# Optimization experiments

Hardware: AMD Instinct MI355X
Metric: run time of the kernel (lower is better)

Reference implementation:

```python
import jax, jax.numpy as jnp
import numpy as np

N_E = 1024
E_DIM = 256
DECAY = 0.99
BETA = 1.0
EPS = 1e-5


def setup_inputs() -> dict:
    key = jax.random.key(0)
    k1, k2, k3 = jax.random.split(key, 3)
    z = jax.random.normal(k1, (32, E_DIM, 64, 64), dtype=jnp.float32)
    embedding = jax.random.normal(k2, (N_E, E_DIM), dtype=jnp.float32)
    embedding_avg = embedding  # buffers initialized as clone of embedding
    cluster_size = jnp.ones((N_E,), dtype=jnp.float32)
    return {"z": z, "embedding": embedding, "embedding_avg": embedding_avg,
            "cluster_size": cluster_size}


def reference(z, embedding, embedding_avg, cluster_size):
    B, C, H, W = z.shape
    zp = jnp.transpose(z, (0, 2, 3, 1))          # [B,H,W,C]
    zf = zp.reshape(-1, C)                        # [N,C]

    # squared euclidean distances [N, n_e]
    d = (jnp.sum(zf * zf, axis=1, keepdims=True)
         + jnp.sum(embedding * embedding, axis=1)[None, :]
         - 2.0 * zf @ embedding.T)
    idx = jnp.argmin(d, axis=1)                   # [N]

    z_q = embedding[idx].reshape(zp.shape)        # [B,H,W,C] (old codebook)

    # training-mode EMA update (scatter-based accumulation)
    counts = jnp.zeros((N_E,), dtype=zf.dtype).at[idx].add(1.0)
    emb_sum = jnp.zeros((N_E, C), dtype=zf.dtype).at[idx].add(zf)
    new_cluster_size = cluster_size * DECAY + (1.0 - DECAY) * counts
    new_embedding_avg = embedding_avg * DECAY + (1.0 - DECAY) * emb_sum
    n = jnp.sum(new_cluster_size)
    smoothed = (new_cluster_size + EPS) / (n + N_E * EPS) * n
    new_embedding = new_embedding_avg / smoothed[:, None]

    sg = jax.lax.stop_gradient
    loss = (BETA * jnp.mean((sg(z_q) - zp) ** 2)
            + jnp.mean((z_q - sg(zp)) ** 2))

    z_q_st = zp + sg(z_q - zp)                    # straight-through
    z_q_out = jnp.transpose(z_q_st, (0, 3, 1, 2))  # back to NCHW
    min_encoding_indices = idx.reshape(B, H, W)
    return (z_q_out, loss, min_encoding_indices,
            new_embedding, new_embedding_avg, new_cluster_size)
```

## Files before the change

### kernel.cpp

```cpp
#include <hip/hip_runtime.h>

#define BATCH 32
#define CDIM 256
#define HW 4096
#define NVEC 131072
#define NE 1024
#define DECAY 0.99f
#define ONE_MINUS_DECAY 0.01f
#define EPSV 1e-5f
#define ZQ_ELEMS 33554432
#define MARGIN 0.02f

typedef _Float16 half8 __attribute__((ext_vector_type(8)));
typedef _Float16 half4 __attribute__((ext_vector_type(4)));
typedef float    f32x4 __attribute__((ext_vector_type(4)));

__global__ __launch_bounds__(256) void prep_half_kernel(
    const float* __restrict__ emb, _Float16* __restrict__ embH,
    _Float16* __restrict__ embL) {
  int i = blockIdx.x * 256 + threadIdx.x;
  float4 v = ((const float4*)emb)[i];
  float x[4] = {v.x, v.y, v.z, v.w};
  half4 hv, lv;
  #pragma unroll
  for (int j = 0; j < 4; ++j) {
    _Float16 h = (_Float16)x[j];
    hv[j] = h;
    lv[j] = (_Float16)(x[j] - (float)h);
  }
  *(half4*)(embH + 4 * (size_t)i) = hv;
  *(half4*)(embL + 4 * (size_t)i) = lv;
}

__global__ __launch_bounds__(256) void enorm_kernel(
    const float* __restrict__ emb, float* __restrict__ enorm) {
  int gid  = blockIdx.x * 256 + threadIdx.x;
  int e    = gid >> 6;
  int lane = threadIdx.x & 63;
  const float4* row = (const float4*)(emb + ((size_t)e << 8));
  float4 v = row[lane];
  float s = v.x * v.x + v.y * v.y + v.z * v.z + v.w * v.w;
  #pragma unroll
  for (int off = 32; off > 0; off >>= 1) s += __shfl_down(s, off);
  if (lane == 0) enorm[e] = s;
}

__global__ __launch_bounds__(512, 2) void argmin_kernel(
    const float* __restrict__ z, const _Float16* __restrict__ embH,
    const _Float16* __restrict__ embL, const float* __restrict__ enorm,
    int* __restrict__ idx_ws, float* __restrict__ idx_out,
    float* __restrict__ counts, int* __restrict__ flag_cnt,
    int* __restrict__ flag_list) {
  __shared__ char smem[65536];

  const int t = threadIdx.x;
  const int w = t >> 6;
  const int l = t & 63;
  const int g = l >> 4;
  const int c = l & 15;
  const int wn = w >> 2;
  const int we = w & 3;

  const int n0  = blockIdx.x * 64;
  const int b   = n0 >> 12;
  const int hw0 = n0 & 4095;
  const float* zb = z + ((size_t)b << 20) + hw0;

  {
    const int n  = t & 63;
    const int kg = t >> 6;
    char* zhp = smem;
    char* zlp = smem + 32768;
    #pragma unroll
    for (int it = 0; it < 4; ++it) {
      const int k0 = it * 64 + kg * 8;
      half8 hv, lv;
      #pragma unroll
      for (int j = 0; j < 8; ++j) {
        float x = zb[(size_t)(k0 + j) * HW + n];
        _Float16 h = (_Float16)x;
        hv[j] = h;
        lv[j] = (_Float16)(x - (float)h);
      }
      const int slot = ((k0 >> 3) ^ (n & 31)) & 31;
      const int byte = n * 512 + slot * 16;
      *(half8*)(zhp + byte) = hv;
      *(half8*)(zlp + byte) = lv;
    }
  }
  __syncthreads();

  float bd[2][4];
  int   bi[2][4];
  unsigned amb = 0u;
  #pragma unroll
  for (int mi = 0; mi < 2; ++mi)
    #pragma unroll
    for (int r = 0; r < 4; ++r) { bd[mi][r] = 3.0e38f; bi[mi][r] = 0; }

  int arow[2], axor[2];
  #pragma unroll
  for (int mi = 0; mi < 2; ++mi) {
    int rowm = 32 * wn + 16 * mi + c;
    arow[mi] = rowm * 512;
    axor[mi] = rowm & 31;
  }

  const char* bhp = (const char*)embH;
  const char* blp = (const char*)embL;

  #pragma unroll 1
  for (int et = 0; et < 4; ++et) {
    const int ebase = et * 256 + we * 64;
    f32x4 acc[2][4];
    #pragma unroll
    for (int mi = 0; mi < 2; ++mi)
      #pragma unroll
      for (int ni = 0; ni < 4; ++ni) {
        f32x4 zr = {0.0f, 0.0f, 0.0f, 0.0f};
        acc[mi][ni] = zr;
      }

    int boff[4];
    #pragma unroll
    for (int ni = 0; ni < 4; ++ni) {
      int eg = ebase + 16 * ni + c;
      boff[ni] = eg * 512 + g * 16;
    }

    #pragma unroll 2
    for (int kc = 0; kc < 256; kc += 32) {
      half8 ah[2], al[2];
      const int kslot = (kc >> 3) + g;
      #pragma unroll
      for (int mi = 0; mi < 2; ++mi) {
        int byte = arow[mi] + (((kslot ^ axor[mi]) & 31) << 4);
        ah[mi] = *(const half8*)(smem + byte);
        al[mi] = *(const half8*)(smem + 32768 + byte);
      }
      #pragma unroll
      for (int nh = 0; nh < 2; ++nh) {
        half8 bh0, bl0, bh1, bl1;
        {
          int o0 = boff[2 * nh]     + kc * 2;
          int o1 = boff[2 * nh + 1] + kc * 2;
          bh0 = *(const half8*)(bhp + o0);
          bl0 = *(const half8*)(blp + o0);
          bh1 = *(const half8*)(bhp + o1);
          bl1 = *(const half8*)(blp + o1);
        }
        #pragma unroll
        for (int mi = 0; mi < 2; ++mi) {
          acc[mi][2*nh]   = __builtin_amdgcn_mfma_f32_16x16x32_f16(ah[mi], bh0, acc[mi][2*nh],   0, 0, 0);
          acc[mi][2*nh]   = __builtin_amdgcn_mfma_f32_16x16x32_f16(ah[mi], bl0, acc[mi][2*nh],   0, 0, 0);
          acc[mi][2*nh]   = __builtin_amdgcn_mfma_f32_16x16x32_f16(al[mi], bh0, acc[mi][2*nh],   0, 0, 0);
          acc[mi][2*nh+1] = __builtin_amdgcn_mfma_f32_16x16x32_f16(ah[mi], bh1, acc[mi][2*nh+1], 0, 0, 0);
          acc[mi][2*nh+1] = __builtin_amdgcn_mfma_f32_16x16x32_f16(ah[mi], bl1, acc[mi][2*nh+1], 0, 0, 0);
          acc[mi][2*nh+1] = __builtin_amdgcn_mfma_f32_16x16x32_f16(al[mi], bh1, acc[mi][2*nh+1], 0, 0, 0);
        }
      }
    }

    #pragma unroll
    for (int ni = 0; ni < 4; ++ni) {
      const int e = ebase + 16 * ni + c;
      const float en = enorm[e];
      #pragma unroll
      for (int mi = 0; mi < 2; ++mi)
        #pragma unroll
        for (int r = 0; r < 4; ++r) {
          const unsigned bit = 1u << (mi * 4 + r);
          float old = bd[mi][r];
          float d = en - 2.0f * acc[mi][ni][r];
          bool better = d < old;
          bool nearr  = fabsf(d - old) < MARGIN;
          if (better) { bd[mi][r] = d; bi[mi][r] = e; }
          unsigned nb = better ? (nearr ? bit : 0u)
                               : ((amb & bit) | (nearr ? bit : 0u));
          amb = (amb & ~bit) | nb;
        }
    }
  }

  #pragma unroll
  for (int off = 1; off < 16; off <<= 1) {
    unsigned oamb = __shfl_xor(amb, off);
    unsigned namb = 0u;
    #pragma unroll
    for (int mi = 0; mi < 2; ++mi)
      #pragma unroll
      for (int r = 0; r < 4; ++r) {
        const unsigned bit = 1u << (mi * 4 + r);
        float od = __shfl_xor(bd[mi][r], off);
        int   oi = __shfl_xor(bi[mi][r], off);
        bool nearr = fabsf(od - bd[mi][r]) < MARGIN;
        bool ow = (od < bd[mi][r]) || (od == bd[mi][r] && oi < bi[mi][r]);
        unsigned sel = ow ? (oamb & bit) : (amb & bit);
        if (ow) { bd[mi][r] = od; bi[mi][r] = oi; }
        if (nearr) sel |= bit;
        namb |= sel;
      }
    amb = namb;
  }

  __syncthreads();
  float* sd = (float*)smem;
  int*   si = (int*)(smem + 1024);
  int*   sa = (int*)(smem + 2048);
  if (c == 0) {
    #pragma unroll
    for (int mi = 0; mi < 2; ++mi)
      #pragma unroll
      for (int r = 0; r < 4; ++r) {
        int nloc = 16 * mi + 4 * g + r;
        sd[w * 32 + nloc] = bd[mi][r];
        si[w * 32 + nloc] = bi[mi][r];
        sa[w * 32 + nloc] = (int)((amb >> (mi * 4 + r)) & 1u);
      }
  }
  __syncthreads();
  if (t < 64) {
    const int half = t >> 5;
    const int rloc = t & 31;
    const int base = half * 128 + rloc;
    float d = sd[base]; int i = si[base]; int a = sa[base];
    #pragma unroll
    for (int j = 1; j < 4; ++j) {
      float od = sd[base + j * 32];
      int   oi = si[base + j * 32];
      int   oa = sa[base + j * 32];
      bool nearr = fabsf(od - d) < MARGIN;
      bool ow = (od < d) || (od == d && oi < i);
      a = (ow ? oa : a) | (nearr ? 1 : 0);
      if (ow) { d = od; i = oi; }
    }
    const int n = n0 + t;
    idx_ws[n]  = i;
    idx_out[n] = (float)i;
    atomicAdd(&counts[i], 1.0f);
    if (a) {
      int p = atomicAdd(flag_cnt, 1);
      flag_list[p] = n;
    }
  }
}

__global__ __launch_bounds__(256) void fixup_kernel(
    const float* __restrict__ z, const float* __restrict__ emb,
    const float* __restrict__ enorm, const int* __restrict__ flag_cnt,
    const int* __restrict__ flag_list, int* __restrict__ idx_ws,
    float* __restrict__ idx_out, float* __restrict__ counts) {
  __shared__ float zf[256];
  __shared__ float rd[256];
  __shared__ int   ri[256];
  const int t = threadIdx.x;
  const int cnt = *flag_cnt;
  for (int fi = blockIdx.x; fi < cnt; fi += gridDim.x) {
    const int n = flag_list[fi];
    const int b = n >> 12, hw = n & 4095;
    __syncthreads();
    zf[t] = z[((size_t)b << 20) + ((size_t)t << 12) + hw];
    __syncthreads();
    float bdv = 3.0e38f; int biv = 0;
    #pragma unroll 1
    for (int rep = 0; rep < 4; ++rep) {
      const int e = rep * 256 + t;
      const float4* er = (const float4*)(emb + ((size_t)e << 8));
      const float4* zr = (const float4*)zf;
      float d0 = 0.f, d1 = 0.f, d2 = 0.f, d3 = 0.f;
      #pragma unroll 8
      for (int k4 = 0; k4 < 64; ++k4) {
        float4 ev = er[k4];
        float4 zv = zr[k4];
        d0 = fmaf(ev.x, zv.x, d0);
        d1 = fmaf(ev.y, zv.y, d1);
        d2 = fmaf(ev.z, zv.z, d2);
        d3 = fmaf(ev.w, zv.w, d3);
      }
      float d = enorm[e] - 2.0f * ((d0 + d1) + (d2 + d3));
      if (d < bdv) { bdv = d; biv = e; }
    }
    rd[t] = bdv; ri[t] = biv;
    __syncthreads();
    for (int s = 128; s > 0; s >>= 1) {
      if (t < s) {
        float od = rd[t + s]; int oi = ri[t + s];
        if (od < rd[t] || (od == rd[t] && oi < ri[t])) { rd[t] = od; ri[t] = oi; }
      }
      __syncthreads();
    }
    if (t == 0) {
      const int nw  = ri[0];
      const int old = idx_ws[n];
      if (nw != old) {
        atomicAdd(&counts[old], -1.0f);
        atomicAdd(&counts[nw],  1.0f);
        idx_ws[n]  = nw;
        idx_out[n] = (float)nw;
      }
    }
    __syncthreads();
  }
}

__global__ __launch_bounds__(256) void fused_scatter_kernel(
    const float* __restrict__ z, const float* __restrict__ emb,
    const int* __restrict__ idx_ws, float* __restrict__ zq_out,
    float* __restrict__ loss_acc, float* __restrict__ emb_sum) {
  __shared__ float hist[NE];
  int t = threadIdx.x;
  #pragma unroll
  for (int i = t; i < NE; i += 256) hist[i] = 0.0f;
  __syncthreads();

  int c     = blockIdx.x & 255;
  int chunk = blockIdx.x >> 8;
  int base  = chunk << 14;

  float lsum = 0.0f;
  const int4* idx4 = (const int4*)idx_ws;
  for (int i4 = t; i4 < 4096; i4 += 256) {
    int n0 = base + (i4 << 2);
    int b  = n0 >> 12;
    int hw = n0 & 4095;
    size_t off = (((size_t)(b << 8) + c) << 12) + hw;
    float4 v = *(const float4*)(z + off);
    int4 id = idx4[n0 >> 2];
    float4 q;
    q.x = emb[((size_t)id.x << 8) + c];
    q.y = emb[((size_t)id.y << 8) + c];
    q.z = emb[((size_t)id.z << 8) + c];
    q.w = emb[((size_t)id.w << 8) + c];
    *(float4*)(zq_out + off) = q;
    float dx = q.x - v.x, dy = q.y - v.y, dz = q.z - v.z, dw = q.w - v.w;
    lsum += dx * dx + dy * dy + dz * dz + dw * dw;
    atomicAdd(&hist[id.x], v.x);
    atomicAdd(&hist[id.y], v.y);
    atomicAdd(&hist[id.z], v.z);
    atomicAdd(&hist[id.w], v.w);
  }
  __syncthreads();

  for (int e = t; e < NE; e += 256)
    atomicAdd(&emb_sum[(e << 8) + c], hist[e]);

  __shared__ float red[256];
  red[t] = lsum;
  __syncthreads();
  for (int s = 128; s > 0; s >>= 1) {
    if (t < s) red[t] += red[t + s];
    __syncthreads();
  }
  if (t == 0) atomicAdd(loss_acc, red[0]);
}

__global__ __launch_bounds__(1024) void ema_cs_kernel(
    const float* __restrict__ cs, const float* __restrict__ counts,
    float* __restrict__ out_ncs, float* __restrict__ n_ws,
    const float* __restrict__ loss_acc, float* __restrict__ loss_out) {
  int e = threadIdx.x;
  float ncs = cs[e] * DECAY + ONE_MINUS_DECAY * counts[e];
  out_ncs[e] = ncs;
  __shared__ float red[1024];
  red[e] = ncs;
  __syncthreads();
  for (int s = 512; s > 0; s >>= 1) {
    if (e < s) red[e] += red[e + s];
    __syncthreads();
  }
  if (e == 0) {
    n_ws[0] = red[0];
    loss_out[0] = loss_acc[0] * 2.0f / (float)ZQ_ELEMS;
  }
}

__global__ __launch_bounds__(256) void ema_emb_kernel(
    const float* __restrict__ eavg, const float* __restrict__ emb_sum,
    const float* __restrict__ ncs, const float* __restrict__ n_ws,
    float* __restrict__ out_eavg, float* __restrict__ out_emb) {
  int i = blockIdx.x * 256 + threadIdx.x;
  int e = i >> 8;
  float ea = eavg[i] * DECAY + ONE_MINUS_DECAY * emb_sum[i];
  out_eavg[i] = ea;
  float nv   = n_ws[0];
  float ncse = ncs[e];
  float sm   = (ncse + EPSV) / (nv + (float)NE * EPSV) * nv;
  out_emb[i] = ea / sm;
}

extern "C" void kernel_launch(void* const* d_in, const int* in_sizes, int n_in,
                              void* d_out, int out_size, void* d_ws, size_t ws_size,
                              hipStream_t stream) {
  const float* z    = (const float*)d_in[0];
  const float* emb  = (const float*)d_in[1];
  const float* eavg = (const float*)d_in[2];
  const float* cs   = (const float*)d_in[3];

  float* out = (float*)d_out;
  float* out_zq   = out;
  float* out_loss = out + 33554432;
  float* out_idx  = out + 33554433;
  float* out_emb  = out + 33685505;
  float* out_eavg = out + 33947649;
  float* out_ncs  = out + 34209793;

  float* ws       = (float*)d_ws;
  int*   idx_ws   = (int*)ws;
  float* emb_sum  = ws + 131072;
  float* counts   = ws + 393216;
  float* loss_acc = ws + 394240;
  float* n_ws     = ws + 394241;
  float* enorm    = ws + 394244;

  _Float16* embH  = (_Float16*)out_zq;
  _Float16* embL  = (_Float16*)(out_zq + 131072);
  int* flag_cnt   = (int*)(out_zq + 262144);
  int* flag_list  = (int*)(out_zq + 262145);

  hipMemsetAsync(ws + 131072, 0, (size_t)263170 * sizeof(float), stream);
  hipMemsetAsync(out_zq + 262144, 0, sizeof(int), stream);

  prep_half_kernel<<<256, 256, 0, stream>>>(emb, embH, embL);
  enorm_kernel<<<NE / 4, 256, 0, stream>>>(emb, enorm);
  argmin_kernel<<<NVEC / 64, 512, 0, stream>>>(z, embH, embL, enorm, idx_ws,
                                               out_idx, counts, flag_cnt, flag_list);
  fixup_kernel<<<1024, 256, 0, stream>>>(z, emb, enorm, flag_cnt, flag_list,
                                         idx_ws, out_idx, counts);
  fused_scatter_kernel<<<2048, 256, 0, stream>>>(z, emb, idx_ws, out_zq, loss_acc, emb_sum);
  ema_cs_kernel<<<1, 1024, 0, stream>>>(cs, counts, out_ncs, n_ws, loss_acc, out_loss);
  ema_emb_kernel<<<262144 / 256, 256, 0, stream>>>(eavg, emb_sum, out_ncs, n_ws, out_eavg, out_emb);
}
```

Measured before the change: 931.9 us.

## Software-pipeline distance GEMM loads with double-buffered registers and narrower per-wave tiles

Restructures the distance GEMM inner loop so each wave covers 32 codewords per pass over 8 passes instead of 64 codewords over 4 passes. Operand fragments from LDS and global memory are double-buffered in registers, so the loads for the next k-chunk are issued before the MFMAs for the current one. The aim is to hide load latency behind MFMA work and to cut accumulator register pressure. In exchange, the A fragments are reloaded from LDS twice as often per codeword, and the argmin epilogue runs more times.

```diff
diff --git a/kernel.cpp b/kernel.cpp
--- a/kernel.cpp
+++ b/kernel.cpp
@@ -109,60 +109,70 @@
   const char* bhp = (const char*)embH;
   const char* blp = (const char*)embL;
 
+#define LOADA(B, kc) {                                              \
+    const int kslot = ((kc) >> 3) + g;                              \
+    int by0 = arow[0] + (((kslot ^ axor[0]) & 31) << 4);            \
+    int by1 = arow[1] + (((kslot ^ axor[1]) & 31) << 4);            \
+    pah[B][0] = *(const half8*)(smem + by0);                        \
+    pal[B][0] = *(const half8*)(smem + 32768 + by0);                \
+    pah[B][1] = *(const half8*)(smem + by1);                        \
+    pal[B][1] = *(const half8*)(smem + 32768 + by1);                \
+  }
+#define LOADB(B, kc) {                                              \
+    int o0 = boff[0] + (kc) * 2;                                    \
+    int o1 = boff[1] + (kc) * 2;                                    \
+    pbh[B][0] = *(const half8*)(bhp + o0);                          \
+    pbl[B][0] = *(const half8*)(blp + o0);                          \
+    pbh[B][1] = *(const half8*)(bhp + o1);                          \
+    pbl[B][1] = *(const half8*)(blp + o1);                          \
+  }
+#define DOMFMA(B) {                                                 \
+    _Pragma("unroll")                                               \
+    for (int mi = 0; mi < 2; ++mi) {                                \
+      _Pragma("unroll")                                             \
+      for (int ni = 0; ni < 2; ++ni) {                              \
+        acc[mi][ni] = __builtin_amdgcn_mfma_f32_16x16x32_f16(pah[B][mi], pbh[B][ni], acc[mi][ni], 0, 0, 0); \
+        acc[mi][ni] = __builtin_amdgcn_mfma_f32_16x16x32_f16(pah[B][mi], pbl[B][ni], acc[mi][ni], 0, 0, 0); \
+        acc[mi][ni] = __builtin_amdgcn_mfma_f32_16x16x32_f16(pal[B][mi], pbh[B][ni], acc[mi][ni], 0, 0, 0); \
+      }                                                             \
+    }                                                               \
+  }
+
   #pragma unroll 1
-  for (int et = 0; et < 4; ++et) {
-    const int ebase = et * 256 + we * 64;
-    f32x4 acc[2][4];
+  for (int p = 0; p < 8; ++p) {
+    const int ebase = p * 128 + we * 32;
+    f32x4 acc[2][2];
     #pragma unroll
     for (int mi = 0; mi < 2; ++mi)
       #pragma unroll
-      for (int ni = 0; ni < 4; ++ni) {
+      for (int ni = 0; ni < 2; ++ni) {
         f32x4 zr = {0.0f, 0.0f, 0.0f, 0.0f};
         acc[mi][ni] = zr;
       }
 
-    int boff[4];
-    #pragma unroll
-    for (int ni = 0; ni < 4; ++ni) {
+    int boff[2];
+    #pragma unroll
+    for (int ni = 0; ni < 2; ++ni) {
       int eg = ebase + 16 * ni + c;
       boff[ni] = eg * 512 + g * 16;
     }
 
-    #pragma unroll 2
-    for (int kc = 0; kc < 256; kc += 32) {
-      half8 ah[2], al[2];
-      const int kslot = (kc >> 3) + g;
-      #pragma unroll
-      for (int mi = 0; mi < 2; ++mi) {
-        int byte = arow[mi] + (((kslot ^ axor[mi]) & 31) << 4);
-        ah[mi] = *(const half8*)(smem + byte);
-        al[mi] = *(const half8*)(smem + 32768 + byte);
-      }
-      #pragma unroll
-      for (int nh = 0; nh < 2; ++nh) {
-        half8 bh0, bl0, bh1, bl1;
-        {
-          int o0 = boff[2 * nh]     + kc * 2;
-          int o1 = boff[2 * nh + 1] + kc * 2;
-          bh0 = *(const half8*)(bhp + o0);
-          bl0 = *(const half8*)(blp + o0);
-          bh1 = *(const half8*)(bhp + o1);
-          bl1 = *(const half8*)(blp + o1);
-        }
-        #pragma unroll
-        for (int mi = 0; mi < 2; ++mi) {
-          acc[mi][2*nh]   = __builtin_amdgcn_mfma_f32_16x16x32_f16(ah[mi], bh0, acc[mi][2*nh],   0, 0, 0);
-          acc[mi][2*nh]   = __builtin_amdgcn_mfma_f32_16x16x32_f16(ah[mi], bl0, acc[mi][2*nh],   0, 0, 0);
-          acc[mi][2*nh]   = __builtin_amdgcn_mfma_f32_16x16x32_f16(al[mi], bh0, acc[mi][2*nh],   0, 0, 0);
-          acc[mi][2*nh+1] = __builtin_amdgcn_mfma_f32_16x16x32_f16(ah[mi], bh1, acc[mi][2*nh+1], 0, 0, 0);
-          acc[mi][2*nh+1] = __builtin_amdgcn_mfma_f32_16x16x32_f16(ah[mi], bl1, acc[mi][2*nh+1], 0, 0, 0);
-          acc[mi][2*nh+1] = __builtin_amdgcn_mfma_f32_16x16x32_f16(al[mi], bh1, acc[mi][2*nh+1], 0, 0, 0);
-        }
-      }
-    }
-
-    #pragma unroll
-    for (int ni = 0; ni < 4; ++ni) {
+    half8 pah[2][2], pal[2][2], pbh[2][2], pbl[2][2];
+
+    LOADA(0, 0) LOADB(0, 0)
+    #pragma unroll 1
+    for (int kc = 0; kc < 192; kc += 64) {
+      LOADA(1, kc + 32) LOADB(1, kc + 32)
+      DOMFMA(0)
+      LOADA(0, kc + 64) LOADB(0, kc + 64)
+      DOMFMA(1)
+    }
+    LOADA(1, 224) LOADB(1, 224)
+    DOMFMA(0)
+    DOMFMA(1)
+
+    #pragma unroll
+    for (int ni = 0; ni < 2; ++ni) {
       const int e = ebase + 16 * ni + c;
       const float en = enorm[e];
       #pragma unroll
@@ -181,6 +191,9 @@
         }
     }
   }
+#undef LOADA
+#undef LOADB
+#undef DOMFMA
 
   #pragma unroll
   for (int off = 1; off < 16; off <<= 1) {
```

Measured after the change: 960.3 us. 3.1% more time.
